# Performance work log

Measured on AMD Instinct MI355X. Metric: run time of the kernel, lower is better.

Reference implementation:

```python
import jax, jax.numpy as jnp
import numpy as np

D_MODEL = 1024
NUM_HEADS = 16
HEAD_DIM = D_MODEL // NUM_HEADS


def setup_inputs() -> dict:
    key = jax.random.key(0)
    ks = jax.random.split(key, 9)
    B, S = 4, 2048
    bound = 1.0 / np.sqrt(D_MODEL)  # nn.Linear default init range
    def lin(kw, kb):
        W = jax.random.uniform(kw, (D_MODEL, D_MODEL), jnp.float32, -bound, bound)
        b = jax.random.uniform(kb, (D_MODEL,), jnp.float32, -bound, bound)
        return W, b
    Wq, bq = lin(ks[0], ks[1])
    Wk, bk = lin(ks[2], ks[3])
    Wv, bv = lin(ks[4], ks[5])
    Wo, bo = lin(ks[6], ks[7])
    x = jax.random.normal(ks[8], (B, S, D_MODEL), jnp.float32)
    return {"x": x, "Wq": Wq, "bq": bq, "Wk": Wk, "bk": bk,
            "Wv": Wv, "bv": bv, "Wo": Wo, "bo": bo}


def reference(x, Wq, bq, Wk, bk, Wv, bv, Wo, bo):
    B, S, _ = x.shape
    scale = 1.0 / np.sqrt(HEAD_DIM)
    # projections; torch Linear is x @ W.T + b; here W stored as [in, out]-style [d,d] already transposed
    def split_heads(t):
        return t.reshape(B, S, NUM_HEADS, HEAD_DIM).transpose(0, 2, 1, 3)  # [B,H,S,Dh]
    q = split_heads(x @ Wq + bq)
    k = split_heads(x @ Wk + bk)
    v = split_heads(x @ Wv + bv)
    scores = jnp.einsum('bhqd,bhkd->bhqk', q, k) * scale  # [B,H,S,S]
    attn = jax.nn.softmax(scores, axis=-1)
    out = jnp.einsum('bhqk,bhkd->bhqd', attn, v)  # [B,H,S,Dh]
    out = out.transpose(0, 2, 1, 3).reshape(B, S, D_MODEL)
    return out @ Wo + bo
```

## Files before the change

### kernel.cpp

```cpp
#include <hip/hip_runtime.h>
#include <hip/hip_bf16.h>

typedef __attribute__((ext_vector_type(8))) short short8;
typedef __attribute__((ext_vector_type(4))) float f32x4;
typedef __attribute__((ext_vector_type(16))) float f32x16;

#define MFMA16(a, b, c) __builtin_amdgcn_mfma_f32_16x16x32_bf16((a), (b), (c), 0, 0, 0)
#define MFMA32(a, b, c) __builtin_amdgcn_mfma_f32_32x32x16_bf16((a), (b), (c), 0, 0, 0)

__device__ __forceinline__ void gload_lds16(const void* g, void* l) {
  __builtin_amdgcn_global_load_lds(
      (const __attribute__((address_space(1))) unsigned int*)g,
      (__attribute__((address_space(3))) unsigned int*)l, 16, 0, 0);
}

__global__ __launch_bounds__(256) void cvt_x(const float* __restrict__ x,
                                             __hip_bfloat16* __restrict__ xb) {
  size_t i = ((size_t)blockIdx.x * 256 + threadIdx.x) * 8;
  float4 a = *(const float4*)(x + i);
  float4 b = *(const float4*)(x + i + 4);
  struct alignas(16) B8 { __hip_bfloat16 h[8]; } o;
  o.h[0] = __float2bfloat16(a.x); o.h[1] = __float2bfloat16(a.y);
  o.h[2] = __float2bfloat16(a.z); o.h[3] = __float2bfloat16(a.w);
  o.h[4] = __float2bfloat16(b.x); o.h[5] = __float2bfloat16(b.y);
  o.h[6] = __float2bfloat16(b.z); o.h[7] = __float2bfloat16(b.w);
  *(B8*)(xb + i) = o;
}

__global__ __launch_bounds__(256) void trans_w(const float* __restrict__ W0,
                                               const float* __restrict__ W1,
                                               const float* __restrict__ W2,
                                               const float* __restrict__ W3,
                                               __hip_bfloat16* __restrict__ Wt) {
  const int which = blockIdx.z;
  const float* W = (which == 0) ? W0 : (which == 1) ? W1 : (which == 2) ? W2 : W3;
  __hip_bfloat16* O = Wt + (size_t)which * 1024 * 1024;
  __shared__ __hip_bfloat16 lds[64][65];
  const int k0 = blockIdx.y * 64, n0 = blockIdx.x * 64;
#pragma unroll
  for (int i = 0; i < 16; ++i) {
    int idx = threadIdx.x + i * 256;
    int r = idx >> 6, c = idx & 63;
    lds[r][c] = __float2bfloat16(W[(size_t)(k0 + r) * 1024 + n0 + c]);
  }
  __syncthreads();
#pragma unroll
  for (int i = 0; i < 16; ++i) {
    int idx = threadIdx.x + i * 256;
    int r = idx >> 6, c = idx & 63;
    O[(size_t)(n0 + r) * 1024 + k0 + c] = lds[c][r];
  }
}

__global__ __launch_bounds__(256) void gemm_qkv(const __hip_bfloat16* __restrict__ A,
                                                const __hip_bfloat16* __restrict__ Wt,
                                                const float* __restrict__ bq,
                                                const float* __restrict__ bk,
                                                const float* __restrict__ bv,
                                                __hip_bfloat16* __restrict__ Qb,
                                                __hip_bfloat16* __restrict__ Kb,
                                                __hip_bfloat16* __restrict__ Vtb) {
  __shared__ __hip_bfloat16 Asm[3][128 * 32];
  __shared__ __hip_bfloat16 Bsm[3][128 * 32];
  const int t = threadIdx.x;
  const int lane = t & 63, w = t >> 6, g = lane >> 4;
  const int bid = (blockIdx.x & 7) * 192 + (blockIdx.x >> 3);
  const int mb0 = (bid / 24) * 128;
  const int nbg = (bid % 24) * 128;
  const int which = nbg >> 10;
  const int nb0 = nbg & 1023;
  const __hip_bfloat16* Bt = Wt + (size_t)which * 1048576;
  const float* bias = (which == 0) ? bq : (which == 1) ? bk : bv;
  const int wr = (w >> 1) * 64, wc = (w & 1) * 64;
  f32x4 acc[4][4] = {};

  const int srow0 = t >> 2;
  const int ssl0 = (t & 3) ^ ((srow0 >> 1) & 3);
  const int srow1 = (t >> 2) + 64;
  const int ssl1 = (t & 3) ^ ((srow1 >> 1) & 3);
  const __hip_bfloat16* Ag0 = A + (size_t)(mb0 + srow0) * 1024 + ssl0 * 8;
  const __hip_bfloat16* Ag1 = A + (size_t)(mb0 + srow1) * 1024 + ssl1 * 8;
  const __hip_bfloat16* Bg0 = Bt + (size_t)(nb0 + srow0) * 1024 + ssl0 * 8;
  const __hip_bfloat16* Bg1 = Bt + (size_t)(nb0 + srow1) * 1024 + ssl1 * 8;
  const int ldst = (t * 16);
  char* wA0 = (char*)&Asm[0][0]; char* wB0 = (char*)&Bsm[0][0];
  char* wA1 = (char*)&Asm[1][0]; char* wB1 = (char*)&Bsm[1][0];
  char* wA2 = (char*)&Asm[2][0]; char* wB2 = (char*)&Bsm[2][0];

#define STAGE_TO(pA, pB, k0n)                                \
  do {                                                       \
    gload_lds16(Ag0 + (k0n), pA + ldst);                     \
    gload_lds16(Ag1 + (k0n), pA + 4096 + ldst);              \
    gload_lds16(Bg0 + (k0n), pB + ldst);                     \
    gload_lds16(Bg1 + (k0n), pB + 4096 + ldst);              \
  } while (0)

#define COMPUTE_FROM(rA, rB)                                                     \
  do {                                                                           \
    short8 a[4], b[4];                                                           \
    _Pragma("unroll") for (int m = 0; m < 4; ++m) {                              \
      int row = wr + m * 16 + (lane & 15);                                       \
      a[m] = *(const short8*)(rA + row * 64 + ((g ^ ((row >> 1) & 3)) * 16));    \
    }                                                                            \
    _Pragma("unroll") for (int n = 0; n < 4; ++n) {                              \
      int row = wc + n * 16 + (lane & 15);                                       \
      b[n] = *(const short8*)(rB + row * 64 + ((g ^ ((row >> 1) & 3)) * 16));    \
    }                                                                            \
    _Pragma("unroll") for (int m = 0; m < 4; ++m)                                \
      _Pragma("unroll") for (int n = 0; n < 4; ++n)                              \
        acc[m][n] = MFMA16(a[m], b[n], acc[m][n]);                               \
  } while (0)

  STAGE_TO(wA0, wB0, 0);
  STAGE_TO(wA1, wB1, 32);
  asm volatile("s_waitcnt vmcnt(4)" ::: "memory");
  __syncthreads();

  for (int u = 0; u < 30; ++u) {
    COMPUTE_FROM(wA0, wB0);
    STAGE_TO(wA2, wB2, (u + 2) * 32);
    asm volatile("s_waitcnt vmcnt(4)" ::: "memory");
    __syncthreads();
    char* tA = wA0; wA0 = wA1; wA1 = wA2; wA2 = tA;
    char* tB = wB0; wB0 = wB1; wB1 = wB2; wB2 = tB;
  }
  COMPUTE_FROM(wA0, wB0);
  asm volatile("s_waitcnt vmcnt(0)" ::: "memory");
  __syncthreads();
  COMPUTE_FROM(wA1, wB1);

#undef STAGE_TO
#undef COMPUTE_FROM

#pragma unroll
  for (int n = 0; n < 4; ++n) {
    int col = nb0 + wc + n * 16 + (lane & 15);
    float bvv = bias[col];
#pragma unroll
    for (int m = 0; m < 4; ++m) {
#pragma unroll
      for (int r = 0; r < 4; ++r) {
        int row = mb0 + wr + m * 16 + g * 4 + r;
        __hip_bfloat16 hv = __float2bfloat16(acc[m][n][r] + bvv);
        if (which == 2) {
          int bb = row >> 11, s = row & 2047;
          int sp = (s & ~12) | ((s & 4) << 1) | ((s & 8) >> 1);
          Vtb[((size_t)(bb * 1024 + col) << 11) + sp] = hv;
        } else {
          __hip_bfloat16* O = which ? Kb : Qb;
          O[(size_t)row * 1024 + col] = hv;
        }
      }
    }
  }
}

__global__ __launch_bounds__(256) void gemm_o(const __hip_bfloat16* __restrict__ A,
                                              const __hip_bfloat16* __restrict__ Bt,
                                              const float* __restrict__ bias,
                                              float* __restrict__ outp) {
  __shared__ __hip_bfloat16 Asm[3][128 * 32];
  __shared__ __hip_bfloat16 Bsm[3][128 * 32];
  const int t = threadIdx.x;
  const int lane = t & 63, w = t >> 6, g = lane >> 4;
  const int bid = (blockIdx.x & 7) * 64 + (blockIdx.x >> 3);
  const int mb0 = (bid / 8) * 128;
  const int nb0 = (bid % 8) * 128;
  const int wr = (w >> 1) * 64, wc = (w & 1) * 64;
  f32x4 acc[4][4] = {};

  const int srow0 = t >> 2;
  const int ssl0 = (t & 3) ^ ((srow0 >> 1) & 3);
  const int srow1 = (t >> 2) + 64;
  const int ssl1 = (t & 3) ^ ((srow1 >> 1) & 3);
  const __hip_bfloat16* Ag0 = A + (size_t)(mb0 + srow0) * 1024 + ssl0 * 8;
  const __hip_bfloat16* Ag1 = A + (size_t)(mb0 + srow1) * 1024 + ssl1 * 8;
  const __hip_bfloat16* Bg0 = Bt + (size_t)(nb0 + srow0) * 1024 + ssl0 * 8;
  const __hip_bfloat16* Bg1 = Bt + (size_t)(nb0 + srow1) * 1024 + ssl1 * 8;
  const int ldst = (t * 16);
  char* wA0 = (char*)&Asm[0][0]; char* wB0 = (char*)&Bsm[0][0];
  char* wA1 = (char*)&Asm[1][0]; char* wB1 = (char*)&Bsm[1][0];
  char* wA2 = (char*)&Asm[2][0]; char* wB2 = (char*)&Bsm[2][0];

#define STAGE_TO(pA, pB, k0n)                                \
  do {                                                       \
    gload_lds16(Ag0 + (k0n), pA + ldst);                     \
    gload_lds16(Ag1 + (k0n), pA + 4096 + ldst);              \
    gload_lds16(Bg0 + (k0n), pB + ldst);                     \
    gload_lds16(Bg1 + (k0n), pB + 4096 + ldst);              \
  } while (0)

#define COMPUTE_FROM(rA, rB)                                                     \
  do {                                                                           \
    short8 a[4], b[4];                                                           \
    _Pragma("unroll") for (int m = 0; m < 4; ++m) {                              \
      int row = wr + m * 16 + (lane & 15);                                       \
      a[m] = *(const short8*)(rA + row * 64 + ((g ^ ((row >> 1) & 3)) * 16));    \
    }                                                                            \
    _Pragma("unroll") for (int n = 0; n < 4; ++n) {                              \
      int row = wc + n * 16 + (lane & 15);                                       \
      b[n] = *(const short8*)(rB + row * 64 + ((g ^ ((row >> 1) & 3)) * 16));    \
    }                                                                            \
    _Pragma("unroll") for (int m = 0; m < 4; ++m)                                \
      _Pragma("unroll") for (int n = 0; n < 4; ++n)                              \
        acc[m][n] = MFMA16(a[m], b[n], acc[m][n]);                               \
  } while (0)

  STAGE_TO(wA0, wB0, 0);
  STAGE_TO(wA1, wB1, 32);
  asm volatile("s_waitcnt vmcnt(4)" ::: "memory");
  __syncthreads();

  for (int u = 0; u < 30; ++u) {
    COMPUTE_FROM(wA0, wB0);
    STAGE_TO(wA2, wB2, (u + 2) * 32);
    asm volatile("s_waitcnt vmcnt(4)" ::: "memory");
    __syncthreads();
    char* tA = wA0; wA0 = wA1; wA1 = wA2; wA2 = tA;
    char* tB = wB0; wB0 = wB1; wB1 = wB2; wB2 = tB;
  }
  COMPUTE_FROM(wA0, wB0);
  asm volatile("s_waitcnt vmcnt(0)" ::: "memory");
  __syncthreads();
  COMPUTE_FROM(wA1, wB1);

#undef STAGE_TO
#undef COMPUTE_FROM

#pragma unroll
  for (int n = 0; n < 4; ++n) {
    int col = nb0 + wc + n * 16 + (lane & 15);
    float bvv = bias[col];
#pragma unroll
    for (int m = 0; m < 4; ++m)
#pragma unroll
      for (int r = 0; r < 4; ++r) {
        int row = mb0 + wr + m * 16 + g * 4 + r;
        outp[(size_t)row * 1024 + col] = acc[m][n][r] + bvv;
      }
  }
}

__global__ __launch_bounds__(256, 2) void attn_fwd8(const __hip_bfloat16* __restrict__ Q,
                                                    const __hip_bfloat16* __restrict__ Kg,
                                                    const __hip_bfloat16* __restrict__ Vt,
                                                    __hip_bfloat16* __restrict__ ctx) {
  __shared__ __hip_bfloat16 Ksm[2][64 * 64];
  __shared__ __hip_bfloat16 Vsm[2][64 * 64];
  const int t = threadIdx.x, lane = t & 63, w = t >> 6;
  const int l31 = lane & 31, hi = lane >> 5;
  const int bid = (blockIdx.x & 7) * 64 + (blockIdx.x >> 3);
  const int bh = bid >> 3, qt = bid & 7;
  const int b = bh >> 4, h = bh & 15;
  const int qA = qt * 256 + w * 64 + l31;

  short8 qfA[4], qfB[4];
  {
    const __hip_bfloat16* qp = Q + ((size_t)(b * 2048 + qA)) * 1024 + h * 64 + hi * 8;
#pragma unroll
    for (int c = 0; c < 4; ++c) qfA[c] = *(const short8*)(qp + 16 * c);
    qp += 32 * 1024;
#pragma unroll
    for (int c = 0; c < 4; ++c) qfB[c] = *(const short8*)(qp + 16 * c);
  }
  const __hip_bfloat16* Kbh = Kg + (size_t)b * 2048 * 1024 + h * 64;
  const __hip_bfloat16* Vbh = Vt + (size_t)(b * 16 + h) * 64 * 2048;

  const int srow = t >> 3;
  const int sslot = t & 7;

#define STAGE(buf, ktn)                                                          \
  do {                                                                           \
    _Pragma("unroll") for (int i = 0; i < 2; ++i) {                              \
      int row = i * 32 + srow;                                                   \
      int sl = sslot ^ (row & 7);                                                \
      gload_lds16(Kbh + (size_t)((ktn) + row) * 1024 + sl * 8,                   \
                  (char*)&Ksm[buf][0] + i * 4096 + w * 1024);                    \
      gload_lds16(Vbh + (size_t)row * 2048 + (ktn) + sl * 8,                     \
                  (char*)&Vsm[buf][0] + i * 4096 + w * 1024);                    \
    }                                                                            \
  } while (0)

  f32x16 otA0 = {}, otA1 = {}, otB0 = {}, otB1 = {};
  float lsA0 = 0.f, lsA1 = 0.f, lsB0 = 0.f, lsB1 = 0.f;
  const float CL = 0.18033688011112042f;
  const float NEG = -43.28085122666891f;

  STAGE(0, 0);
  asm volatile("s_waitcnt vmcnt(0)" ::: "memory");
  __syncthreads();

  for (int kt = 0; kt < 2048; kt += 64) {
    const int cur = (kt >> 6) & 1;
    if (kt + 64 < 2048) STAGE(cur ^ 1, kt + 64);

    const char* Kb0 = (const char*)&Ksm[cur][0];
    const char* Vb0 = (const char*)&Vsm[cur][0];

    f32x16 sA0 = {}, sA1 = {}, sB0 = {}, sB1 = {};
    {
      short8 kf[2][4];
#pragma unroll
      for (int s = 0; s < 2; ++s)
#pragma unroll
        for (int c = 0; c < 4; ++c) {
          int row = s * 32 + l31;
          kf[s][c] = *(const short8*)(Kb0 + row * 128 + (((hi + 2 * c) ^ (row & 7)) * 16));
        }
#pragma unroll
      for (int c = 0; c < 4; ++c) {
        sA0 = MFMA32(kf[0][c], qfA[c], sA0);
        sA1 = MFMA32(kf[1][c], qfA[c], sA1);
        sB0 = MFMA32(kf[0][c], qfB[c], sB0);
        sB1 = MFMA32(kf[1][c], qfB[c], sB1);
      }
    }

    short8 vf[2][4];
#pragma unroll
    for (int dt = 0; dt < 2; ++dt)
#pragma unroll
      for (int c = 0; c < 4; ++c) {
        int row = dt * 32 + l31;
        vf[dt][c] = *(const short8*)(Vb0 + row * 128 + (((hi + 2 * c) ^ (row & 7)) * 16));
      }

    {
      unsigned ua[16];
#pragma unroll
      for (int n = 0; n < 8; ++n) {
        float a0 = __builtin_fmaf(sA0[2 * n], CL, NEG);
        float a1 = __builtin_fmaf(sA0[2 * n + 1], CL, NEG);
        float e0, e1;
        asm("v_exp_f32 %0, %1" : "=v"(e0) : "v"(a0));
        asm("v_exp_f32 %0, %1" : "=v"(e1) : "v"(a1));
        lsA0 += e0; lsA1 += e1;
        asm("v_cvt_pk_bf16_f32 %0, %1, %2" : "=v"(ua[n]) : "v"(e0), "v"(e1));
      }
#pragma unroll
      for (int n = 0; n < 8; ++n) {
        float a0 = __builtin_fmaf(sA1[2 * n], CL, NEG);
        float a1 = __builtin_fmaf(sA1[2 * n + 1], CL, NEG);
        float e0, e1;
        asm("v_exp_f32 %0, %1" : "=v"(e0) : "v"(a0));
        asm("v_exp_f32 %0, %1" : "=v"(e1) : "v"(a1));
        lsA0 += e0; lsA1 += e1;
        asm("v_cvt_pk_bf16_f32 %0, %1, %2" : "=v"(ua[8 + n]) : "v"(e0), "v"(e1));
      }
#pragma unroll
      for (int c = 0; c < 4; ++c) {
        union { unsigned u[4]; short8 s8; } pb;
        pb.u[0] = ua[4 * c]; pb.u[1] = ua[4 * c + 1];
        pb.u[2] = ua[4 * c + 2]; pb.u[3] = ua[4 * c + 3];
        otA0 = MFMA32(vf[0][c], pb.s8, otA0);
        otA1 = MFMA32(vf[1][c], pb.s8, otA1);
      }
    }

    {
      unsigned ub[16];
#pragma unroll
      for (int n = 0; n < 8; ++n) {
        float a0 = __builtin_fmaf(sB0[2 * n], CL, NEG);
        float a1 = __builtin_fmaf(sB0[2 * n + 1], CL, NEG);
        float e0, e1;
        asm("v_exp_f32 %0, %1" : "=v"(e0) : "v"(a0));
        asm("v_exp_f32 %0, %1" : "=v"(e1) : "v"(a1));
        lsB0 += e0; lsB1 += e1;
        asm("v_cvt_pk_bf16_f32 %0, %1, %2" : "=v"(ub[n]) : "v"(e0), "v"(e1));
      }
#pragma unroll
      for (int n = 0; n < 8; ++n) {
        float a0 = __builtin_fmaf(sB1[2 * n], CL, NEG);
        float a1 = __builtin_fmaf(sB1[2 * n + 1], CL, NEG);
        float e0, e1;
        asm("v_exp_f32 %0, %1" : "=v"(e0) : "v"(a0));
        asm("v_exp_f32 %0, %1" : "=v"(e1) : "v"(a1));
        lsB0 += e0; lsB1 += e1;
        asm("v_cvt_pk_bf16_f32 %0, %1, %2" : "=v"(ub[8 + n]) : "v"(e0), "v"(e1));
      }
#pragma unroll
      for (int c = 0; c < 4; ++c) {
        union { unsigned u[4]; short8 s8; } pb;
        pb.u[0] = ub[4 * c]; pb.u[1] = ub[4 * c + 1];
        pb.u[2] = ub[4 * c + 2]; pb.u[3] = ub[4 * c + 3];
        otB0 = MFMA32(vf[0][c], pb.s8, otB0);
        otB1 = MFMA32(vf[1][c], pb.s8, otB1);
      }
    }

    asm volatile("s_waitcnt vmcnt(0)" ::: "memory");
    __syncthreads();
  }
#undef STAGE

  float lsumA = lsA0 + lsA1;
  lsumA += __shfl_xor(lsumA, 32);
  float invA = 1.0f / lsumA;
  float lsumB = lsB0 + lsB1;
  lsumB += __shfl_xor(lsumB, 32);
  float invB = 1.0f / lsumB;

  {
    __hip_bfloat16* op = ctx + ((size_t)(b * 2048 + qA)) * 1024 + h * 64 + 4 * hi;
#pragma unroll
    for (int dt = 0; dt < 2; ++dt) {
#pragma unroll
      for (int g = 0; g < 4; ++g) {
        struct alignas(8) H4 { __hip_bfloat16 x[4]; } o4;
#pragma unroll
        for (int e = 0; e < 4; ++e)
          o4.x[e] = __float2bfloat16((dt ? otA1[4 * g + e] : otA0[4 * g + e]) * invA);
        *(H4*)(op + 32 * dt + 8 * g) = o4;
      }
    }
    op += 32 * 1024;
#pragma unroll
    for (int dt = 0; dt < 2; ++dt) {
#pragma unroll
      for (int g = 0; g < 4; ++g) {
        struct alignas(8) H4 { __hip_bfloat16 x[4]; } o4;
#pragma unroll
        for (int e = 0; e < 4; ++e)
          o4.x[e] = __float2bfloat16((dt ? otB1[4 * g + e] : otB0[4 * g + e]) * invB);
        *(H4*)(op + 32 * dt + 8 * g) = o4;
      }
    }
  }
}

extern "C" void kernel_launch(void* const* d_in, const int* in_sizes, int n_in,
                              void* d_out, int out_size, void* d_ws, size_t ws_size,
                              hipStream_t stream) {
  (void)in_sizes; (void)n_in; (void)out_size; (void)ws_size;
  const float* x  = (const float*)d_in[0];
  const float* Wq = (const float*)d_in[1];
  const float* bq = (const float*)d_in[2];
  const float* Wk = (const float*)d_in[3];
  const float* bk = (const float*)d_in[4];
  const float* Wv = (const float*)d_in[5];
  const float* bv = (const float*)d_in[6];
  const float* Wo = (const float*)d_in[7];
  const float* bo = (const float*)d_in[8];
  float* out = (float*)d_out;

  __hip_bfloat16* ws  = (__hip_bfloat16*)d_ws;
  __hip_bfloat16* xb  = ws;
  __hip_bfloat16* Wt  = xb + 8388608;
  __hip_bfloat16* Qb  = Wt + 4194304;
  __hip_bfloat16* Kb  = Qb + 8388608;
  __hip_bfloat16* Vtb = Kb + 8388608;
  __hip_bfloat16* ctx = xb;

  cvt_x<<<4096, 256, 0, stream>>>(x, xb);
  trans_w<<<dim3(16, 16, 4), 256, 0, stream>>>(Wq, Wk, Wv, Wo, Wt);
  gemm_qkv<<<1536, 256, 0, stream>>>(xb, Wt, bq, bk, bv, Qb, Kb, Vtb);
  attn_fwd8<<<512, 256, 0, stream>>>(Qb, Kb, Vtb, ctx);
  gemm_o<<<512, 256, 0, stream>>>(ctx, Wt + 3145728, bo, out);
}
```

Before: 216.6 us.

## Rewrite QKV GEMM with 256x256 tiles, 8 waves, BK=64 double buffering

```diff
diff --git a/kernel.cpp b/kernel.cpp
--- a/kernel.cpp
+++ b/kernel.cpp
@@ -52,7 +52,7 @@
   }
 }
 
-__global__ __launch_bounds__(256) void gemm_qkv(const __hip_bfloat16* __restrict__ A,
+__global__ __launch_bounds__(512) void gemm_qkv(const __hip_bfloat16* __restrict__ A,
                                                 const __hip_bfloat16* __restrict__ Wt,
                                                 const float* __restrict__ bq,
                                                 const float* __restrict__ bk,
@@ -60,17 +60,114 @@
                                                 __hip_bfloat16* __restrict__ Qb,
                                                 __hip_bfloat16* __restrict__ Kb,
                                                 __hip_bfloat16* __restrict__ Vtb) {
+  __shared__ __hip_bfloat16 Asm[2][256 * 64];
+  __shared__ __hip_bfloat16 Bsm[2][256 * 64];
+  const int t = threadIdx.x;
+  const int lane = t & 63, w = t >> 6;
+  const int l15 = lane & 15, g = lane >> 4;
+  const int wm = (w >> 2) * 128;
+  const int wn = (w & 3) * 64;
+  const int bid = (blockIdx.x & 7) * 48 + (blockIdx.x >> 3);
+  const int mb0 = (bid / 12) * 256;
+  const int nbg = (bid % 12) * 256;
+  const int which = nbg >> 10;
+  const int nb0 = nbg & 1023;
+  const __hip_bfloat16* Bt = Wt + (size_t)which * 1048576;
+  const float* bias = (which == 0) ? bq : (which == 1) ? bk : bv;
+  f32x4 acc[8][4] = {};
+
+  const int srow = t >> 3;
+  const int ssl = (t & 7) ^ (srow & 7);
+  const __hip_bfloat16* Ags = A + (size_t)(mb0 + srow) * 1024 + ssl * 8;
+  const __hip_bfloat16* Bgs = Bt + (size_t)(nb0 + srow) * 1024 + ssl * 8;
+
+#define STAGE_TILE(bufi, k0n)                                          \
+  do {                                                                 \
+    _Pragma("unroll") for (int uu = 0; uu < 4; ++uu) {                 \
+      gload_lds16(Ags + (size_t)uu * 65536 + (k0n),                    \
+                  (char*)&Asm[bufi][0] + uu * 8192 + t * 16);          \
+      gload_lds16(Bgs + (size_t)uu * 65536 + (k0n),                    \
+                  (char*)&Bsm[bufi][0] + uu * 8192 + t * 16);          \
+    }                                                                  \
+  } while (0)
+
+#define QUAD(cA, cB, mh, nh)                                                     \
+  do {                                                                           \
+    short8 af[4][2], bf[2][2];                                                   \
+    _Pragma("unroll") for (int mi = 0; mi < 4; ++mi) {                           \
+      int row = wm + ((mh) * 4 + mi) * 16 + l15;                                 \
+      _Pragma("unroll") for (int kk = 0; kk < 2; ++kk)                           \
+        af[mi][kk] = *(const short8*)((cA) + row * 128 +                         \
+                                      (((kk * 4 + g) ^ (row & 7)) * 16));        \
+    }                                                                            \
+    _Pragma("unroll") for (int ni = 0; ni < 2; ++ni) {                           \
+      int row = wn + ((nh) * 2 + ni) * 16 + l15;                                 \
+      _Pragma("unroll") for (int kk = 0; kk < 2; ++kk)                           \
+        bf[ni][kk] = *(const short8*)((cB) + row * 128 +                         \
+                                      (((kk * 4 + g) ^ (row & 7)) * 16));        \
+    }                                                                            \
+    __builtin_amdgcn_s_barrier();                                                \
+    _Pragma("unroll") for (int mi = 0; mi < 4; ++mi)                             \
+      _Pragma("unroll") for (int ni = 0; ni < 2; ++ni)                           \
+        _Pragma("unroll") for (int kk = 0; kk < 2; ++kk)                         \
+          acc[(mh) * 4 + mi][(nh) * 2 + ni] =                                    \
+              MFMA16(af[mi][kk], bf[ni][kk], acc[(mh) * 4 + mi][(nh) * 2 + ni]); \
+    __builtin_amdgcn_s_barrier();                                                \
+  } while (0)
+
+  STAGE_TILE(0, 0);
+  asm volatile("s_waitcnt vmcnt(0)" ::: "memory");
+  __builtin_amdgcn_s_barrier();
+
+  for (int u = 0; u < 16; ++u) {
+    const int cur = u & 1;
+    const char* cA = (const char*)&Asm[cur][0];
+    const char* cB = (const char*)&Bsm[cur][0];
+    if (u < 15) STAGE_TILE(cur ^ 1, (u + 1) * 64);
+    QUAD(cA, cB, 0, 0);
+    QUAD(cA, cB, 0, 1);
+    QUAD(cA, cB, 1, 0);
+    QUAD(cA, cB, 1, 1);
+    asm volatile("s_waitcnt vmcnt(0)" ::: "memory");
+    __builtin_amdgcn_s_barrier();
+  }
+#undef STAGE_TILE
+#undef QUAD
+
+#pragma unroll
+  for (int ni = 0; ni < 4; ++ni) {
+    int col = nb0 + wn + ni * 16 + l15;
+    float bvv = bias[col];
+#pragma unroll
+    for (int mi = 0; mi < 8; ++mi) {
+#pragma unroll
+      for (int r = 0; r < 4; ++r) {
+        int row = mb0 + wm + mi * 16 + g * 4 + r;
+        __hip_bfloat16 hv = __float2bfloat16(acc[mi][ni][r] + bvv);
+        if (which == 2) {
+          int bb = row >> 11, s = row & 2047;
+          int sp = (s & ~12) | ((s & 4) << 1) | ((s & 8) >> 1);
+          Vtb[((size_t)(bb * 1024 + col) << 11) + sp] = hv;
+        } else {
+          __hip_bfloat16* O = which ? Kb : Qb;
+          O[(size_t)row * 1024 + col] = hv;
+        }
+      }
+    }
+  }
+}
+
+__global__ __launch_bounds__(256) void gemm_o(const __hip_bfloat16* __restrict__ A,
+                                              const __hip_bfloat16* __restrict__ Bt,
+                                              const float* __restrict__ bias,
+                                              float* __restrict__ outp) {
   __shared__ __hip_bfloat16 Asm[3][128 * 32];
   __shared__ __hip_bfloat16 Bsm[3][128 * 32];
   const int t = threadIdx.x;
   const int lane = t & 63, w = t >> 6, g = lane >> 4;
-  const int bid = (blockIdx.x & 7) * 192 + (blockIdx.x >> 3);
-  const int mb0 = (bid / 24) * 128;
-  const int nbg = (bid % 24) * 128;
-  const int which = nbg >> 10;
-  const int nb0 = nbg & 1023;
-  const __hip_bfloat16* Bt = Wt + (size_t)which * 1048576;
-  const float* bias = (which == 0) ? bq : (which == 1) ? bk : bv;
+  const int bid = (blockIdx.x & 7) * 64 + (blockIdx.x >> 3);
+  const int mb0 = (bid / 8) * 128;
+  const int nb0 = (bid % 8) * 128;
   const int wr = (w >> 1) * 64, wc = (w & 1) * 64;
   f32x4 acc[4][4] = {};
 
@@ -137,101 +234,6 @@
     int col = nb0 + wc + n * 16 + (lane & 15);
     float bvv = bias[col];
 #pragma unroll
-    for (int m = 0; m < 4; ++m) {
-#pragma unroll
-      for (int r = 0; r < 4; ++r) {
-        int row = mb0 + wr + m * 16 + g * 4 + r;
-        __hip_bfloat16 hv = __float2bfloat16(acc[m][n][r] + bvv);
-        if (which == 2) {
-          int bb = row >> 11, s = row & 2047;
-          int sp = (s & ~12) | ((s & 4) << 1) | ((s & 8) >> 1);
-          Vtb[((size_t)(bb * 1024 + col) << 11) + sp] = hv;
-        } else {
-          __hip_bfloat16* O = which ? Kb : Qb;
-          O[(size_t)row * 1024 + col] = hv;
-        }
-      }
-    }
-  }
-}
-
-__global__ __launch_bounds__(256) void gemm_o(const __hip_bfloat16* __restrict__ A,
-                                              const __hip_bfloat16* __restrict__ Bt,
-                                              const float* __restrict__ bias,
-                                              float* __restrict__ outp) {
-  __shared__ __hip_bfloat16 Asm[3][128 * 32];
-  __shared__ __hip_bfloat16 Bsm[3][128 * 32];
-  const int t = threadIdx.x;
-  const int lane = t & 63, w = t >> 6, g = lane >> 4;
-  const int bid = (blockIdx.x & 7) * 64 + (blockIdx.x >> 3);
-  const int mb0 = (bid / 8) * 128;
-  const int nb0 = (bid % 8) * 128;
-  const int wr = (w >> 1) * 64, wc = (w & 1) * 64;
-  f32x4 acc[4][4] = {};
-
-  const int srow0 = t >> 2;
-  const int ssl0 = (t & 3) ^ ((srow0 >> 1) & 3);
-  const int srow1 = (t >> 2) + 64;
-  const int ssl1 = (t & 3) ^ ((srow1 >> 1) & 3);
-  const __hip_bfloat16* Ag0 = A + (size_t)(mb0 + srow0) * 1024 + ssl0 * 8;
-  const __hip_bfloat16* Ag1 = A + (size_t)(mb0 + srow1) * 1024 + ssl1 * 8;
-  const __hip_bfloat16* Bg0 = Bt + (size_t)(nb0 + srow0) * 1024 + ssl0 * 8;
-  const __hip_bfloat16* Bg1 = Bt + (size_t)(nb0 + srow1) * 1024 + ssl1 * 8;
-  const int ldst = (t * 16);
-  char* wA0 = (char*)&Asm[0][0]; char* wB0 = (char*)&Bsm[0][0];
-  char* wA1 = (char*)&Asm[1][0]; char* wB1 = (char*)&Bsm[1][0];
-  char* wA2 = (char*)&Asm[2][0]; char* wB2 = (char*)&Bsm[2][0];
-
-#define STAGE_TO(pA, pB, k0n)                                \
-  do {                                                       \
-    gload_lds16(Ag0 + (k0n), pA + ldst);                     \
-    gload_lds16(Ag1 + (k0n), pA + 4096 + ldst);              \
-    gload_lds16(Bg0 + (k0n), pB + ldst);                     \
-    gload_lds16(Bg1 + (k0n), pB + 4096 + ldst);              \
-  } while (0)
-
-#define COMPUTE_FROM(rA, rB)                                                     \
-  do {                                                                           \
-    short8 a[4], b[4];                                                           \
-    _Pragma("unroll") for (int m = 0; m < 4; ++m) {                              \
-      int row = wr + m * 16 + (lane & 15);                                       \
-      a[m] = *(const short8*)(rA + row * 64 + ((g ^ ((row >> 1) & 3)) * 16));    \
-    }                                                                            \
-    _Pragma("unroll") for (int n = 0; n < 4; ++n) {                              \
-      int row = wc + n * 16 + (lane & 15);                                       \
-      b[n] = *(const short8*)(rB + row * 64 + ((g ^ ((row >> 1) & 3)) * 16));    \
-    }                                                                            \
-    _Pragma("unroll") for (int m = 0; m < 4; ++m)                                \
-      _Pragma("unroll") for (int n = 0; n < 4; ++n)                              \
-        acc[m][n] = MFMA16(a[m], b[n], acc[m][n]);                               \
-  } while (0)
-
-  STAGE_TO(wA0, wB0, 0);
-  STAGE_TO(wA1, wB1, 32);
-  asm volatile("s_waitcnt vmcnt(4)" ::: "memory");
-  __syncthreads();
-
-  for (int u = 0; u < 30; ++u) {
-    COMPUTE_FROM(wA0, wB0);
-    STAGE_TO(wA2, wB2, (u + 2) * 32);
-    asm volatile("s_waitcnt vmcnt(4)" ::: "memory");
-    __syncthreads();
-    char* tA = wA0; wA0 = wA1; wA1 = wA2; wA2 = tA;
-    char* tB = wB0; wB0 = wB1; wB1 = wB2; wB2 = tB;
-  }
-  COMPUTE_FROM(wA0, wB0);
-  asm volatile("s_waitcnt vmcnt(0)" ::: "memory");
-  __syncthreads();
-  COMPUTE_FROM(wA1, wB1);
-
-#undef STAGE_TO
-#undef COMPUTE_FROM
-
-#pragma unroll
-  for (int n = 0; n < 4; ++n) {
-    int col = nb0 + wc + n * 16 + (lane & 15);
-    float bvv = bias[col];
-#pragma unroll
     for (int m = 0; m < 4; ++m)
 #pragma unroll
       for (int r = 0; r < 4; ++r) {
@@ -454,7 +456,7 @@
 
   cvt_x<<<4096, 256, 0, stream>>>(x, xb);
   trans_w<<<dim3(16, 16, 4), 256, 0, stream>>>(Wq, Wk, Wv, Wo, Wt);
-  gemm_qkv<<<1536, 256, 0, stream>>>(xb, Wt, bq, bk, bv, Qb, Kb, Vtb);
+  gemm_qkv<<<384, 512, 0, stream>>>(xb, Wt, bq, bk, bv, Qb, Kb, Vtb);
   attn_fwd8<<<512, 256, 0, stream>>>(Qb, Kb, Vtb, ctx);
   gemm_o<<<512, 256, 0, stream>>>(ctx, Wt + 3145728, bo, out);
 }
```

Measured after the change: 236.8 us. +9.3%, slower.

## Compute Q, K, V projections in one block sharing the A tile

Applied to the files above, without the earlier changes.

```diff
diff --git a/kernel.cpp b/kernel.cpp
--- a/kernel.cpp
+++ b/kernel.cpp
@@ -60,17 +60,128 @@
                                                 __hip_bfloat16* __restrict__ Qb,
                                                 __hip_bfloat16* __restrict__ Kb,
                                                 __hip_bfloat16* __restrict__ Vtb) {
+  __shared__ __hip_bfloat16 Asm[2][128 * 32];
+  __shared__ __hip_bfloat16 Bsm[3][2][128 * 32];
+  const int t = threadIdx.x;
+  const int lane = t & 63, w = t >> 6, g = lane >> 4;
+  const int bid = (blockIdx.x & 7) * 64 + (blockIdx.x >> 3);
+  const int mb0 = (bid >> 3) * 128;
+  const int nb0 = (bid & 7) * 128;
+  const int wr = (w >> 1) * 64, wc = (w & 1) * 64;
+  f32x4 acc0[4][4] = {}, acc1[4][4] = {}, acc2[4][4] = {};
+
+  const int srow0 = t >> 2;
+  const int ssl0 = (t & 3) ^ ((srow0 >> 1) & 3);
+  const int srow1 = (t >> 2) + 64;
+  const int ssl1 = (t & 3) ^ ((srow1 >> 1) & 3);
+  const __hip_bfloat16* Ag0 = A + (size_t)(mb0 + srow0) * 1024 + ssl0 * 8;
+  const __hip_bfloat16* Ag1 = A + (size_t)(mb0 + srow1) * 1024 + ssl1 * 8;
+  const __hip_bfloat16* Qg0 = Wt + (size_t)(nb0 + srow0) * 1024 + ssl0 * 8;
+  const __hip_bfloat16* Qg1 = Wt + (size_t)(nb0 + srow1) * 1024 + ssl1 * 8;
+  const __hip_bfloat16* Kg0 = Qg0 + 1048576;
+  const __hip_bfloat16* Kg1 = Qg1 + 1048576;
+  const __hip_bfloat16* Vg0 = Qg0 + 2097152;
+  const __hip_bfloat16* Vg1 = Qg1 + 2097152;
+  const int ldst = t * 16;
+  char* aC = (char*)&Asm[0][0];      char* aN = (char*)&Asm[1][0];
+  char* qC = (char*)&Bsm[0][0][0];   char* qN = (char*)&Bsm[0][1][0];
+  char* kC = (char*)&Bsm[1][0][0];   char* kN = (char*)&Bsm[1][1][0];
+  char* vC = (char*)&Bsm[2][0][0];   char* vN = (char*)&Bsm[2][1][0];
+
+#define STAGE_TO(pa, pq, pk, pv, k0n)                        \
+  do {                                                       \
+    gload_lds16(Ag0 + (k0n), (pa) + ldst);                   \
+    gload_lds16(Ag1 + (k0n), (pa) + 4096 + ldst);            \
+    gload_lds16(Qg0 + (k0n), (pq) + ldst);                   \
+    gload_lds16(Qg1 + (k0n), (pq) + 4096 + ldst);            \
+    gload_lds16(Kg0 + (k0n), (pk) + ldst);                   \
+    gload_lds16(Kg1 + (k0n), (pk) + 4096 + ldst);            \
+    gload_lds16(Vg0 + (k0n), (pv) + ldst);                   \
+    gload_lds16(Vg1 + (k0n), (pv) + 4096 + ldst);            \
+  } while (0)
+
+#define RD_B(bf, rB)                                                             \
+  _Pragma("unroll") for (int n = 0; n < 4; ++n) {                                \
+    int row = wc + n * 16 + (lane & 15);                                         \
+    bf[n] = *(const short8*)((rB) + row * 64 + ((g ^ ((row >> 1) & 3)) * 16));   \
+  }
+
+#define MM16(bf, accX)                                                           \
+  _Pragma("unroll") for (int m = 0; m < 4; ++m)                                  \
+    _Pragma("unroll") for (int n = 0; n < 4; ++n)                                \
+      accX[m][n] = MFMA16(a[m], bf[n], accX[m][n]);
+
+  STAGE_TO(aC, qC, kC, vC, 0);
+  asm volatile("s_waitcnt vmcnt(0)" ::: "memory");
+  __syncthreads();
+
+  for (int u = 0; u < 32; ++u) {
+    if (u < 31) STAGE_TO(aN, qN, kN, vN, (u + 1) * 32);
+
+    short8 a[4];
+#pragma unroll
+    for (int m = 0; m < 4; ++m) {
+      int row = wr + m * 16 + (lane & 15);
+      a[m] = *(const short8*)(aC + row * 64 + ((g ^ ((row >> 1) & 3)) * 16));
+    }
+    {
+      short8 b[4];
+      RD_B(b, qC);
+      MM16(b, acc0);
+    }
+    {
+      short8 b[4];
+      RD_B(b, kC);
+      MM16(b, acc1);
+    }
+    {
+      short8 b[4];
+      RD_B(b, vC);
+      MM16(b, acc2);
+    }
+
+    asm volatile("s_waitcnt vmcnt(0)" ::: "memory");
+    __syncthreads();
+    char* tp;
+    tp = aC; aC = aN; aN = tp;
+    tp = qC; qC = qN; qN = tp;
+    tp = kC; kC = kN; kN = tp;
+    tp = vC; vC = vN; vN = tp;
+  }
+#undef STAGE_TO
+#undef RD_B
+#undef MM16
+
+#pragma unroll
+  for (int n = 0; n < 4; ++n) {
+    int col = nb0 + wc + n * 16 + (lane & 15);
+    float bvq = bq[col], bvk = bk[col], bvv = bv[col];
+#pragma unroll
+    for (int m = 0; m < 4; ++m) {
+#pragma unroll
+      for (int r = 0; r < 4; ++r) {
+        int row = mb0 + wr + m * 16 + g * 4 + r;
+        Qb[(size_t)row * 1024 + col] = __float2bfloat16(acc0[m][n][r] + bvq);
+        Kb[(size_t)row * 1024 + col] = __float2bfloat16(acc1[m][n][r] + bvk);
+        int bb = row >> 11, s = row & 2047;
+        int sp = (s & ~12) | ((s & 4) << 1) | ((s & 8) >> 1);
+        Vtb[((size_t)(bb * 1024 + col) << 11) + sp] = __float2bfloat16(acc2[m][n][r] + bvv);
+      }
+    }
+  }
+}
+
+__global__ __launch_bounds__(256) void gemm_o(const __hip_bfloat16* __restrict__ A,
+                                              const __hip_bfloat16* __restrict__ Bt,
+                                              const float* __restrict__ bias,
+                                              float* __restrict__ outp) {
   __shared__ __hip_bfloat16 Asm[3][128 * 32];
   __shared__ __hip_bfloat16 Bsm[3][128 * 32];
   const int t = threadIdx.x;
   const int lane = t & 63, w = t >> 6, g = lane >> 4;
-  const int bid = (blockIdx.x & 7) * 192 + (blockIdx.x >> 3);
-  const int mb0 = (bid / 24) * 128;
-  const int nbg = (bid % 24) * 128;
-  const int which = nbg >> 10;
-  const int nb0 = nbg & 1023;
-  const __hip_bfloat16* Bt = Wt + (size_t)which * 1048576;
-  const float* bias = (which == 0) ? bq : (which == 1) ? bk : bv;
+  const int bid = (blockIdx.x & 7) * 64 + (blockIdx.x >> 3);
+  const int mb0 = (bid / 8) * 128;
+  const int nb0 = (bid % 8) * 128;
   const int wr = (w >> 1) * 64, wc = (w & 1) * 64;
   f32x4 acc[4][4] = {};
 
@@ -120,108 +231,15 @@
     COMPUTE_FROM(wA0, wB0);
     STAGE_TO(wA2, wB2, (u + 2) * 32);
     asm volatile("s_waitcnt vmcnt(4)" ::: "memory");
-    __syncthreads();
+    __builtin_amdgcn_s_barrier();
+    asm volatile("" ::: "memory");
     char* tA = wA0; wA0 = wA1; wA1 = wA2; wA2 = tA;
     char* tB = wB0; wB0 = wB1; wB1 = wB2; wB2 = tB;
   }
   COMPUTE_FROM(wA0, wB0);
   asm volatile("s_waitcnt vmcnt(0)" ::: "memory");
-  __syncthreads();
-  COMPUTE_FROM(wA1, wB1);
-
-#undef STAGE_TO
-#undef COMPUTE_FROM
-
-#pragma unroll
-  for (int n = 0; n < 4; ++n) {
-    int col = nb0 + wc + n * 16 + (lane & 15);
-    float bvv = bias[col];
-#pragma unroll
-    for (int m = 0; m < 4; ++m) {
-#pragma unroll
-      for (int r = 0; r < 4; ++r) {
-        int row = mb0 + wr + m * 16 + g * 4 + r;
-        __hip_bfloat16 hv = __float2bfloat16(acc[m][n][r] + bvv);
-        if (which == 2) {
-          int bb = row >> 11, s = row & 2047;
-          int sp = (s & ~12) | ((s & 4) << 1) | ((s & 8) >> 1);
-          Vtb[((size_t)(bb * 1024 + col) << 11) + sp] = hv;
-        } else {
-          __hip_bfloat16* O = which ? Kb : Qb;
-          O[(size_t)row * 1024 + col] = hv;
-        }
-      }
-    }
-  }
-}
-
-__global__ __launch_bounds__(256) void gemm_o(const __hip_bfloat16* __restrict__ A,
-                                              const __hip_bfloat16* __restrict__ Bt,
-                                              const float* __restrict__ bias,
-                                              float* __restrict__ outp) {
-  __shared__ __hip_bfloat16 Asm[3][128 * 32];
-  __shared__ __hip_bfloat16 Bsm[3][128 * 32];
-  const int t = threadIdx.x;
-  const int lane = t & 63, w = t >> 6, g = lane >> 4;
-  const int bid = (blockIdx.x & 7) * 64 + (blockIdx.x >> 3);
-  const int mb0 = (bid / 8) * 128;
-  const int nb0 = (bid % 8) * 128;
-  const int wr = (w >> 1) * 64, wc = (w & 1) * 64;
-  f32x4 acc[4][4] = {};
-
-  const int srow0 = t >> 2;
-  const int ssl0 = (t & 3) ^ ((srow0 >> 1) & 3);
-  const int srow1 = (t >> 2) + 64;
-  const int ssl1 = (t & 3) ^ ((srow1 >> 1) & 3);
-  const __hip_bfloat16* Ag0 = A + (size_t)(mb0 + srow0) * 1024 + ssl0 * 8;
-  const __hip_bfloat16* Ag1 = A + (size_t)(mb0 + srow1) * 1024 + ssl1 * 8;
-  const __hip_bfloat16* Bg0 = Bt + (size_t)(nb0 + srow0) * 1024 + ssl0 * 8;
-  const __hip_bfloat16* Bg1 = Bt + (size_t)(nb0 + srow1) * 1024 + ssl1 * 8;
-  const int ldst = (t * 16);
-  char* wA0 = (char*)&Asm[0][0]; char* wB0 = (char*)&Bsm[0][0];
-  char* wA1 = (char*)&Asm[1][0]; char* wB1 = (char*)&Bsm[1][0];
-  char* wA2 = (char*)&Asm[2][0]; char* wB2 = (char*)&Bsm[2][0];
-
-#define STAGE_TO(pA, pB, k0n)                                \
-  do {                                                       \
-    gload_lds16(Ag0 + (k0n), pA + ldst);                     \
-    gload_lds16(Ag1 + (k0n), pA + 4096 + ldst);              \
-    gload_lds16(Bg0 + (k0n), pB + ldst);                     \
-    gload_lds16(Bg1 + (k0n), pB + 4096 + ldst);              \
-  } while (0)
-
-#define COMPUTE_FROM(rA, rB)                                                     \
-  do {                                                                           \
-    short8 a[4], b[4];                                                           \
-    _Pragma("unroll") for (int m = 0; m < 4; ++m) {                              \
-      int row = wr + m * 16 + (lane & 15);                                       \
-      a[m] = *(const short8*)(rA + row * 64 + ((g ^ ((row >> 1) & 3)) * 16));    \
-    }                                                                            \
-    _Pragma("unroll") for (int n = 0; n < 4; ++n) {                              \
-      int row = wc + n * 16 + (lane & 15);                                       \
-      b[n] = *(const short8*)(rB + row * 64 + ((g ^ ((row >> 1) & 3)) * 16));    \
-    }                                                                            \
-    _Pragma("unroll") for (int m = 0; m < 4; ++m)                                \
-      _Pragma("unroll") for (int n = 0; n < 4; ++n)                              \
-        acc[m][n] = MFMA16(a[m], b[n], acc[m][n]);                               \
-  } while (0)
-
-  STAGE_TO(wA0, wB0, 0);
-  STAGE_TO(wA1, wB1, 32);
-  asm volatile("s_waitcnt vmcnt(4)" ::: "memory");
-  __syncthreads();
-
-  for (int u = 0; u < 30; ++u) {
-    COMPUTE_FROM(wA0, wB0);
-    STAGE_TO(wA2, wB2, (u + 2) * 32);
-    asm volatile("s_waitcnt vmcnt(4)" ::: "memory");
-    __syncthreads();
-    char* tA = wA0; wA0 = wA1; wA1 = wA2; wA2 = tA;
-    char* tB = wB0; wB0 = wB1; wB1 = wB2; wB2 = tB;
-  }
-  COMPUTE_FROM(wA0, wB0);
-  asm volatile("s_waitcnt vmcnt(0)" ::: "memory");
-  __syncthreads();
+  __builtin_amdgcn_s_barrier();
+  asm volatile("" ::: "memory");
   COMPUTE_FROM(wA1, wB1);
 
 #undef STAGE_TO
@@ -454,7 +472,7 @@
 
   cvt_x<<<4096, 256, 0, stream>>>(x, xb);
   trans_w<<<dim3(16, 16, 4), 256, 0, stream>>>(Wq, Wk, Wv, Wo, Wt);
-  gemm_qkv<<<1536, 256, 0, stream>>>(xb, Wt, bq, bk, bv, Qb, Kb, Vtb);
+  gemm_qkv<<<512, 256, 0, stream>>>(xb, Wt, bq, bk, bv, Qb, Kb, Vtb);
   attn_fwd8<<<512, 256, 0, stream>>>(Qb, Kb, Vtb, ctx);
   gemm_o<<<512, 256, 0, stream>>>(ctx, Wt + 3145728, bo, out);
 }
```

Result: no change. 213.5 us (-1.5%).
